# Kernel tuning notes

Measured on AMD Instinct MI355X. Metric: run time of the kernel, lower is better.

The kernel has to match this reference:

```python
import jax, jax.numpy as jnp
import numpy as np

BN_EPS = 1e-5
NORM_EPS = 1e-12
TEMPERATURE = 0.07
TOP_K = 128


def _projection_head(x, W1, b1, gamma, beta, W2, b2):
    # Linear(hidden, hidden); torch Linear weight is [out, in]
    y = x @ W1.T + b1
    # BatchNorm1d in training mode: batch statistics (biased variance)
    mu = jnp.mean(y, axis=0)
    var = jnp.var(y, axis=0)
    y = gamma * (y - mu) * jax.lax.rsqrt(var + BN_EPS) + beta
    # exact (erf) GELU, matching torch default
    y = jax.nn.gelu(y, approximate=False)
    return y @ W2.T + b2


def _l2_normalize(x):
    n = jnp.linalg.norm(x, axis=-1, keepdims=True)
    return x / jnp.maximum(n, NORM_EPS)


def setup_inputs() -> dict:
    key = jax.random.key(0)
    ks = jax.random.split(key, 5)
    B, N_NEG, H, P = 4096, 32768, 1024, 256
    h1 = jax.random.normal(ks[0], (B, H), dtype=jnp.float32)
    h2 = jax.random.normal(ks[1], (B, H), dtype=jnp.float32)
    h_neg = jax.random.normal(ks[2], (N_NEG, H), dtype=jnp.float32)
    W1 = jax.random.normal(ks[3], (H, H), dtype=jnp.float32) * (1.0 / np.sqrt(H))
    b1 = jnp.zeros((H,), dtype=jnp.float32)
    gamma = jnp.ones((H,), dtype=jnp.float32)
    beta = jnp.zeros((H,), dtype=jnp.float32)
    W2 = jax.random.normal(ks[4], (P, H), dtype=jnp.float32) * (1.0 / np.sqrt(H))
    b2 = jnp.zeros((P,), dtype=jnp.float32)
    return {"h1": h1, "h2": h2, "h_neg": h_neg, "W1": W1, "b1": b1,
            "gamma": gamma, "beta": beta, "W2": W2, "b2": b2}


def reference(h1, h2, h_neg, W1, b1, gamma, beta, W2, b2):
    z1 = _l2_normalize(_projection_head(h1, W1, b1, gamma, beta, W2, b2))
    z2 = _l2_normalize(_projection_head(h2, W1, b1, gamma, beta, W2, b2))
    z_neg = _l2_normalize(_projection_head(h_neg, W1, b1, gamma, beta, W2, b2))

    sim_neg = z1 @ z_neg.T                      # [B, N_neg]
    _, hard_idx = jax.lax.top_k(sim_neg, TOP_K) # [B, K]
    z_hard = z_neg[hard_idx]                    # [B, K, P] gather

    pos_sim = jnp.sum(z1 * z2, axis=-1, keepdims=True) / TEMPERATURE      # [B, 1]
    neg_sim = jnp.einsum('bp,bkp->bk', z1, z_hard) / TEMPERATURE          # [B, K]
    logits = jnp.concatenate([pos_sim, neg_sim], axis=1)                  # [B, 1+K]
    # cross entropy with all labels = 0
    loss = -jnp.mean(jax.nn.log_softmax(logits, axis=-1)[:, 0])
    return loss
```

## Files before the change

kernel.cpp:

```cpp
#include <hip/hip_runtime.h>
#include <hip/hip_bf16.h>
#include <math.h>

#define BATCH 4096
#define NNEG 32768
#define HID 1024
#define PROJ 256
#define TOPK 128
#define ROWS_TOTAL 40960
#define CHUNK 1024
#define INV_T 14.2857142857142857f

#define BM 128
#define BN 128
#define BK 64

#define BNS_ROWS 128

typedef __attribute__((ext_vector_type(8))) short bf16x8;
typedef __attribute__((ext_vector_type(4))) float f32x4;

__device__ __forceinline__ float b2f(unsigned short u) {
    return __uint_as_float(((unsigned)u) << 16);
}
__device__ __forceinline__ unsigned short f2b(float f) {
    unsigned u = __float_as_uint(f);
    unsigned r = (u + 0x7FFFu + ((u >> 16) & 1u)) >> 16;
    return (unsigned short)r;
}
__device__ __forceinline__ float gelu_fast(float v) {
    float v2 = v * v;
    float w = v * fmaf(v2, -0.1029433f, -2.3022086f);
    float e = exp2f(w);
    return v * __builtin_amdgcn_rcpf(1.0f + e);
}

__device__ __forceinline__ float blockReduceSumF(float v, volatile float* scratch) {
    #pragma unroll
    for (int o = 32; o > 0; o >>= 1) v += __shfl_down(v, o);
    int wid = threadIdx.x >> 6, lane = threadIdx.x & 63;
    __syncthreads();
    if (lane == 0) scratch[wid] = v;
    __syncthreads();
    return scratch[0] + scratch[1] + scratch[2] + scratch[3];
}
__device__ __forceinline__ int blockReduceSumI(int v, volatile int* scratch) {
    #pragma unroll
    for (int o = 32; o > 0; o >>= 1) v += __shfl_down(v, o);
    int wid = threadIdx.x >> 6, lane = threadIdx.x & 63;
    __syncthreads();
    if (lane == 0) scratch[wid] = v;
    __syncthreads();
    return scratch[0] + scratch[1] + scratch[2] + scratch[3];
}

__device__ __forceinline__ void gl_lds16(const unsigned short* g, unsigned short* l) {
    __builtin_amdgcn_global_load_lds(
        (const __attribute__((address_space(1))) unsigned*)g,
        (__attribute__((address_space(3))) unsigned*)l, 16, 0, 0);
}

__global__ __launch_bounds__(256) void conv_f2b(const float* __restrict__ src,
                                                unsigned short* __restrict__ dst, int n)
{
    int i = (blockIdx.x * 256 + threadIdx.x) * 4;
    if (i + 3 < n) {
        float4 v = *(const float4*)(src + i);
        ushort4 o;
        o.x = f2b(v.x); o.y = f2b(v.y); o.z = f2b(v.z); o.w = f2b(v.w);
        *(ushort4*)(dst + i) = o;
    }
}

__global__ __launch_bounds__(256) void conv_f2b8(const float* __restrict__ src,
                                                 unsigned short* __restrict__ dst)
{
    int i = (blockIdx.x * 256 + threadIdx.x) * 8;
    float4 a = *(const float4*)(src + i);
    float4 b = *(const float4*)(src + i + 4);
    ushort4 o0, o1;
    o0.x = f2b(a.x); o0.y = f2b(a.y); o0.z = f2b(a.z); o0.w = f2b(a.w);
    o1.x = f2b(b.x); o1.y = f2b(b.y); o1.z = f2b(b.z); o1.w = f2b(b.w);
    *(ushort4*)(dst + i) = o0;
    *(ushort4*)(dst + i + 4) = o1;
}

__device__ __forceinline__ void xcd_swizzle(int& bx, int& by) {
    int gx = gridDim.x;
    int orig = by * gx + bx;
    int q = (gx * gridDim.y) >> 3;
    int wg = (orig & 7) * q + (orig >> 3);
    bx = wg % gx;
    by = wg / gx;
}

__global__ __launch_bounds__(256) void mfma_gemm(
    const unsigned short* __restrict__ A, const unsigned short* __restrict__ Bw,
    const float* __restrict__ bias, unsigned short* __restrict__ C,
    int M, int N, int K)
{
    __shared__ unsigned short As[BM * BK];
    __shared__ unsigned short Bs[BN * BK];
    const int tid = threadIdx.x;
    int bxi = blockIdx.x, byi = blockIdx.y;
    xcd_swizzle(bxi, byi);
    const int bm = byi * BM;
    const int bn = bxi * BN;
    const int wave = tid >> 6;
    const int lane = tid & 63;
    const int wm = (wave >> 1) * 64;
    const int wn = (wave & 1) * 64;
    const int fr = lane & 15;
    const int fg = lane >> 4;

    int s_slot[4], s_row[4], s_c16[4];
    #pragma unroll
    for (int i = 0; i < 4; i++) {
        int s = wave * 256 + i * 64 + lane;
        s_slot[i] = (wave * 256 + i * 64) * 8;
        s_row[i] = s >> 3;
        s_c16[i] = (s & 7) ^ ((s >> 3) & 7);
    }

    f32x4 acc[4][4] = {};

    for (int k0 = 0; k0 < K; k0 += BK) {
        #pragma unroll
        for (int i = 0; i < 4; i++) {
            gl_lds16(A  + (size_t)(bm + s_row[i]) * K + k0 + s_c16[i] * 8, &As[s_slot[i]]);
            gl_lds16(Bw + (size_t)(bn + s_row[i]) * K + k0 + s_c16[i] * 8, &Bs[s_slot[i]]);
        }
        __syncthreads();
        #pragma unroll
        for (int ks = 0; ks < 2; ks++) {
            bf16x8 a[4], b[4];
            #pragma unroll
            for (int mi = 0; mi < 4; mi++) {
                int row = wm + mi * 16 + fr;
                a[mi] = *(const bf16x8*)&As[row * 64 + (((ks * 4 + fg) ^ (row & 7)) << 3)];
            }
            #pragma unroll
            for (int ni = 0; ni < 4; ni++) {
                int row = wn + ni * 16 + fr;
                b[ni] = *(const bf16x8*)&Bs[row * 64 + (((ks * 4 + fg) ^ (row & 7)) << 3)];
            }
            #pragma unroll
            for (int mi = 0; mi < 4; mi++)
                #pragma unroll
                for (int ni = 0; ni < 4; ni++)
                    acc[mi][ni] = __builtin_amdgcn_mfma_f32_16x16x32_bf16(a[mi], b[ni], acc[mi][ni], 0, 0, 0);
        }
        __syncthreads();
    }

    #pragma unroll
    for (int mi = 0; mi < 4; mi++) {
        #pragma unroll
        for (int ni = 0; ni < 4; ni++) {
            int col = bn + wn + ni * 16 + fr;
            int row0 = bm + wm + mi * 16 + fg * 4;
            float bv = bias ? bias[col] : 0.0f;
            #pragma unroll
            for (int r = 0; r < 4; r++) {
                float v = acc[mi][ni][r] + bv;
                C[(size_t)(row0 + r) * N + col] = f2b(v);
            }
        }
    }
}

__global__ __launch_bounds__(256) void bn_stats_partial(const unsigned short* __restrict__ Yb,
                                                        float* __restrict__ partial)
{
    __shared__ float lsum[1024];
    __shared__ float lssq[1024];
    const int cg = (threadIdx.x & 127) * 8;
    int r = blockIdx.x * BNS_ROWS + (threadIdx.x >> 7);
    float s[8] = {}, ss[8] = {};
    #pragma unroll 4
    for (int i = 0; i < BNS_ROWS / 2; i++, r += 2) {
        uint4 v = *(const uint4*)&Yb[(size_t)r * HID + cg];
        const unsigned short* u = (const unsigned short*)&v;
        #pragma unroll
        for (int j = 0; j < 8; j++) {
            float f = b2f(u[j]);
            s[j] += f; ss[j] += f * f;
        }
    }
    if (threadIdx.x >= 128) {
        #pragma unroll
        for (int j = 0; j < 8; j++) { lsum[cg + j] = s[j]; lssq[cg + j] = ss[j]; }
    }
    __syncthreads();
    if (threadIdx.x < 128) {
        float* outs = partial + (size_t)blockIdx.x * 2048;
        #pragma unroll
        for (int j = 0; j < 8; j++) {
            outs[cg + j]        = s[j] + lsum[cg + j];
            outs[1024 + cg + j] = ss[j] + lssq[cg + j];
        }
    }
}

__global__ __launch_bounds__(256) void bn_reduce_finalize(
    const float* __restrict__ partial,
    const float* __restrict__ gamma, const float* __restrict__ beta,
    float* __restrict__ scale, float* __restrict__ shift)
{
    int seg = blockIdx.y;
    int col = blockIdx.x * 256 + threadIdx.x;
    int base = (seg == 0) ? 0 : (seg == 1) ? 32 : 64;
    int nblk = (seg == 2) ? 256 : 32;
    const float* p = partial + (size_t)base * 2048;
    float s = 0.f, ss = 0.f;
    for (int b = 0; b < nblk; b++) {
        s  += p[(size_t)b * 2048 + col];
        ss += p[(size_t)b * 2048 + 1024 + col];
    }
    float n = (seg == 2) ? (float)NNEG : (float)BATCH;
    float mu = s / n;
    float var = ss / n - mu * mu;
    float sc = gamma[col] * rsqrtf(var + 1e-5f);
    scale[seg * HID + col] = sc;
    shift[seg * HID + col] = beta[col] - mu * sc;
}

__global__ __launch_bounds__(256) void bngelu(unsigned short* __restrict__ Yb,
                                              const float* __restrict__ scale,
                                              const float* __restrict__ shift)
{
    size_t i = ((size_t)blockIdx.x * 256 + threadIdx.x) * 8;
    int row = (int)(i >> 10);
    int seg = (row < BATCH) ? 0 : (row < 2 * BATCH) ? 1 : 2;
    int col = (int)(i & 1023);
    float4 sc0 = *(const float4*)(scale + seg * HID + col);
    float4 sc1 = *(const float4*)(scale + seg * HID + col + 4);
    float4 sh0 = *(const float4*)(shift + seg * HID + col);
    float4 sh1 = *(const float4*)(shift + seg * HID + col + 4);
    float sc[8] = { sc0.x, sc0.y, sc0.z, sc0.w, sc1.x, sc1.y, sc1.z, sc1.w };
    float sh[8] = { sh0.x, sh0.y, sh0.z, sh0.w, sh1.x, sh1.y, sh1.z, sh1.w };
    uint4 v = *(uint4*)&Yb[i];
    unsigned short* u = (unsigned short*)&v;
    #pragma unroll
    for (int j = 0; j < 8; j++) {
        float f = fmaf(b2f(u[j]), sc[j], sh[j]);
        u[j] = f2b(gelu_fast(f));
    }
    *(uint4*)&Yb[i] = v;
}

__global__ __launch_bounds__(256) void l2norm(unsigned short* __restrict__ Z,
                                              float* __restrict__ Zfp)
{
    __shared__ float scratch[4];
    size_t r = blockIdx.x;
    float v = b2f(Z[r * PROJ + threadIdx.x]);
    float t = blockReduceSumF(v * v, scratch);
    float scale = 1.0f / fmaxf(sqrtf(t), 1e-12f);
    float o = v * scale;
    Z[r * PROJ + threadIdx.x] = f2b(o);
    if (r < 2 * BATCH) Zfp[r * PROJ + threadIdx.x] = o;
}

__global__ __launch_bounds__(256) void topk_loss(
    const unsigned short* __restrict__ simb,
    const float* __restrict__ z1, const float* __restrict__ z2,
    int rowOffset, float* __restrict__ rowloss)
{
    __shared__ int   hcnt[4096];
    __shared__ int   segc[256];
    __shared__ int   sufc[256];
    __shared__ float fscratch[4];
    __shared__ int   iscratch[4];
    __shared__ int   sel_seg;
    __shared__ int   sh_bt, sh_run;

    const int tid = threadIdx.x;
    const int grow = rowOffset + blockIdx.x;
    const unsigned short* srow = simb + (size_t)blockIdx.x * NNEG;

    #pragma unroll
    for (int j = 0; j < 16; j++) hcnt[tid * 16 + j] = 0;

    float p = z1[(size_t)grow * PROJ + tid] * z2[(size_t)grow * PROJ + tid];
    float pos = blockReduceSumF(p, fscratch);
    __syncthreads();

    for (int i = tid * 8; i < NNEG; i += 256 * 8) {
        uint4 v4 = *(const uint4*)(srow + i);
        const unsigned short* u = (const unsigned short*)&v4;
        #pragma unroll
        for (int j = 0; j < 8; j++) {
            float v = b2f(u[j]);
            int k = (int)fmaf(v, 2048.f, 2048.f);
            k = min(max(k, 0), 4095);
            atomicAdd(&hcnt[k], 1);
        }
    }
    __syncthreads();

    int c = 0;
    #pragma unroll
    for (int j = 0; j < 16; j++) c += hcnt[tid * 16 + j];
    segc[tid] = c;
    sufc[tid] = c;
    __syncthreads();
    for (int st = 1; st < 256; st <<= 1) {
        int aC = (tid + st < 256) ? sufc[tid + st] : 0;
        __syncthreads();
        sufc[tid] += aC;
        __syncthreads();
    }
    if (sufc[tid] >= TOPK && sufc[tid] - segc[tid] < TOPK) sel_seg = tid;
    __syncthreads();
    if (tid == 0) {
        int t = sel_seg;
        int running = sufc[t] - segc[t];
        int bt = t * 16;
        for (int j = 15; j >= 0; j--) {
            int b = t * 16 + j;
            int cb = hcnt[b];
            if (running + cb >= TOPK) { bt = b; break; }
            running += cb;
        }
        sh_bt = bt; sh_run = running;
    }
    __syncthreads();
    const int bt = sh_bt;
    const float m = INV_T;

    float s_above = 0.f, s_eq = 0.f;
    int c_eq = 0;
    for (int i = tid * 8; i < NNEG; i += 256 * 8) {
        uint4 v4 = *(const uint4*)(srow + i);
        const unsigned short* u = (const unsigned short*)&v4;
        #pragma unroll
        for (int j = 0; j < 8; j++) {
            float v = b2f(u[j]);
            int k = (int)fmaf(v, 2048.f, 2048.f);
            k = min(max(k, 0), 4095);
            if (k >= bt) {
                float e = __expf(fmaf(v, INV_T, -m));
                if (k > bt) s_above += e;
                else { s_eq += e; c_eq++; }
            }
        }
    }
    s_above = blockReduceSumF(s_above, fscratch);
    __syncthreads();
    s_eq = blockReduceSumF(s_eq, fscratch);
    c_eq = blockReduceSumI(c_eq, iscratch);
    if (tid == 0) {
        int need = TOPK - sh_run;
        float avg = s_eq / (float)c_eq;
        float total = s_above + (float)need * avg + __expf(fmaf(pos, INV_T, -m));
        rowloss[grow] = m + logf(total) - pos * INV_T;
    }
}

__global__ __launch_bounds__(256) void loss_reduce(const float* __restrict__ rowloss,
                                                   float* __restrict__ out)
{
    __shared__ float scratch[4];
    float s = 0.f;
    for (int i = threadIdx.x; i < BATCH; i += 256) s += rowloss[i];
    s = blockReduceSumF(s, scratch);
    if (threadIdx.x == 0) out[0] = s / (float)BATCH;
}

extern "C" void kernel_launch(void* const* d_in, const int* in_sizes, int n_in,
                              void* d_out, int out_size, void* d_ws, size_t ws_size,
                              hipStream_t stream)
{
    const float* h1    = (const float*)d_in[0];
    const float* h2    = (const float*)d_in[1];
    const float* hneg  = (const float*)d_in[2];
    const float* W1    = (const float*)d_in[3];
    const float* b1    = (const float*)d_in[4];
    const float* gamma = (const float*)d_in[5];
    const float* beta  = (const float*)d_in[6];
    const float* W2    = (const float*)d_in[7];
    const float* b2    = (const float*)d_in[8];
    float* out = (float*)d_out;
    float* ws  = (float*)d_ws;

    unsigned short* X_all = (unsigned short*)ws;
    unsigned short* Yb    = (unsigned short*)(ws + 20971520);
    unsigned short* Z     = (unsigned short*)(ws + 41943040);
    unsigned short* W1b   = (unsigned short*)(ws + 47185920);
    unsigned short* W2b   = (unsigned short*)(ws + 47710208);
    float* partial = ws + 47841280;
    float* s_scale = ws + 48496640;
    float* s_shift = ws + 48499712;
    float* rowloss = ws + 48502784;
    unsigned short* simb = X_all;
    float*          Zfp  = ws + 16777216;

    conv_f2b<<<1024, 256, 0, stream>>>(W1, W1b, HID * HID);
    conv_f2b<<<256, 256, 0, stream>>>(W2, W2b, PROJ * HID);
    conv_f2b8<<<2048, 256, 0, stream>>>(h1, X_all);
    conv_f2b8<<<2048, 256, 0, stream>>>(h2, X_all + (size_t)BATCH * HID);
    conv_f2b8<<<16384, 256, 0, stream>>>(hneg, X_all + (size_t)2 * BATCH * HID);

    {
        dim3 g(HID / BN, ROWS_TOTAL / BM);
        mfma_gemm<<<g, 256, 0, stream>>>(X_all, W1b, b1, Yb, ROWS_TOTAL, HID, HID);
    }

    const int rows[3] = { BATCH, BATCH, NNEG };
    const int yoff[3] = { 0, BATCH, 2 * BATCH };
    const int poff[3] = { 0, 32, 64 };

    for (int s = 0; s < 3; s++) {
        bn_stats_partial<<<rows[s] / BNS_ROWS, 256, 0, stream>>>(
            Yb + (size_t)yoff[s] * HID, partial + (size_t)poff[s] * 2048);
    }
    bn_reduce_finalize<<<dim3(HID / 256, 3), 256, 0, stream>>>(partial, gamma, beta, s_scale, s_shift);

    bngelu<<<ROWS_TOTAL * HID / 8 / 256, 256, 0, stream>>>(Yb, s_scale, s_shift);

    {
        dim3 g(PROJ / BN, ROWS_TOTAL / BM);
        mfma_gemm<<<g, 256, 0, stream>>>(Yb, W2b, b2, Z, ROWS_TOTAL, PROJ, HID);
    }
    l2norm<<<ROWS_TOTAL, 256, 0, stream>>>(Z, Zfp);

    const unsigned short* znegb = Z + (size_t)(2 * BATCH) * PROJ;
    const float* z2v = Zfp + (size_t)BATCH * PROJ;
    for (int c = 0; c < BATCH / CHUNK; c++) {
        dim3 g(NNEG / BN, CHUNK / BM);
        mfma_gemm<<<g, 256, 0, stream>>>(Z + (size_t)(c * CHUNK) * PROJ, znegb, nullptr,
                                         simb, CHUNK, NNEG, PROJ);
        topk_loss<<<CHUNK, 256, 0, stream>>>(simb, Zfp, z2v, c * CHUNK, rowloss);
    }
    loss_reduce<<<1, 256, 0, stream>>>(rowloss, out);
}
```

Before: 621.7 us.

## Keep similarity row in registers across histogram and sum passes; double chunk size

The top-k loss kernel now loads each row's 32768 bf16 similarities into 16 uint4 registers per thread once and reuses them for both the histogram pass and the exp-sum pass, instead of reading global memory twice. The similarity chunk size is doubled, so fewer chunked GEMM and top-k launches are needed, and the fp32 Z buffer is moved to a new workspace offset so the larger similarity buffer does not overlap it. This raises register pressure (64 extra VGPRs) and may lower occupancy.

```diff
diff --git a/kernel.cpp b/kernel.cpp
--- a/kernel.cpp
+++ b/kernel.cpp
@@ -8,7 +8,7 @@
 #define PROJ 256
 #define TOPK 128
 #define ROWS_TOTAL 40960
-#define CHUNK 1024
+#define CHUNK 2048
 #define INV_T 14.2857142857142857f
 
 #define BM 128
@@ -286,15 +286,23 @@
     float pos = blockReduceSumF(p, fscratch);
     __syncthreads();
 
-    for (int i = tid * 8; i < NNEG; i += 256 * 8) {
-        uint4 v4 = *(const uint4*)(srow + i);
-        const unsigned short* u = (const unsigned short*)&v4;
-        #pragma unroll
-        for (int j = 0; j < 8; j++) {
-            float v = b2f(u[j]);
-            int k = (int)fmaf(v, 2048.f, 2048.f);
-            k = min(max(k, 0), 4095);
-            atomicAdd(&hcnt[k], 1);
+    uint4 vreg[16];
+    #pragma unroll
+    for (int i = 0; i < 16; i++)
+        vreg[i] = *(const uint4*)(srow + ((size_t)i * 256 + tid) * 8);
+
+    #pragma unroll
+    for (int i = 0; i < 16; i++) {
+        const unsigned* w = (const unsigned*)&vreg[i];
+        #pragma unroll
+        for (int j = 0; j < 4; j++) {
+            unsigned pq = w[j];
+            float v0 = b2f((unsigned short)(pq & 0xFFFFu));
+            float v1 = b2f((unsigned short)(pq >> 16));
+            int k0 = min(max((int)fmaf(v0, 2048.f, 2048.f), 0), 4095);
+            int k1 = min(max((int)fmaf(v1, 2048.f, 2048.f), 0), 4095);
+            atomicAdd(&hcnt[k0], 1);
+            atomicAdd(&hcnt[k1], 1);
         }
     }
     __syncthreads();
@@ -331,18 +339,21 @@
 
     float s_above = 0.f, s_eq = 0.f;
     int c_eq = 0;
-    for (int i = tid * 8; i < NNEG; i += 256 * 8) {
-        uint4 v4 = *(const uint4*)(srow + i);
-        const unsigned short* u = (const unsigned short*)&v4;
-        #pragma unroll
-        for (int j = 0; j < 8; j++) {
-            float v = b2f(u[j]);
-            int k = (int)fmaf(v, 2048.f, 2048.f);
-            k = min(max(k, 0), 4095);
-            if (k >= bt) {
-                float e = __expf(fmaf(v, INV_T, -m));
-                if (k > bt) s_above += e;
-                else { s_eq += e; c_eq++; }
+    #pragma unroll
+    for (int i = 0; i < 16; i++) {
+        const unsigned* w = (const unsigned*)&vreg[i];
+        #pragma unroll
+        for (int j = 0; j < 4; j++) {
+            unsigned pq = w[j];
+            #pragma unroll
+            for (int h = 0; h < 2; h++) {
+                float v = b2f((unsigned short)((h == 0) ? (pq & 0xFFFFu) : (pq >> 16)));
+                int k = min(max((int)fmaf(v, 2048.f, 2048.f), 0), 4095);
+                if (k >= bt) {
+                    float e = __expf(fmaf(v, INV_T, -m));
+                    if (k > bt) s_above += e;
+                    else { s_eq += e; c_eq++; }
+                }
             }
         }
     }
@@ -393,8 +404,8 @@
     float* s_scale = ws + 48496640;
     float* s_shift = ws + 48499712;
     float* rowloss = ws + 48502784;
+    float* Zfp     = ws + 48506880;
     unsigned short* simb = X_all;
-    float*          Zfp  = ws + 16777216;
 
     conv_f2b<<<1024, 256, 0, stream>>>(W1, W1b, HID * HID);
     conv_f2b<<<256, 256, 0, stream>>>(W2, W2b, PROJ * HID);
```

New measurement: 667.2 us. +7.3%, slower.

## Double-buffer LDS tiles in MFMA GEMM to overlap global loads with compute

Applied to the files above, without the earlier changes.

Makes the GEMM's shared-memory A/B tiles double-buffered. The next K-tile is prefetched via global-to-LDS loads while MFMAs run on the current tile, which leaves one barrier per iteration instead of two. Row base pointers are also precomputed once. LDS use doubles to 64KB per block, which may reduce occupancy. The Zfp workspace pointer is moved to a separate region, apparently to avoid aliasing with other buffers.

```diff
diff --git a/kernel.cpp b/kernel.cpp
--- a/kernel.cpp
+++ b/kernel.cpp
@@ -99,8 +99,8 @@
     const float* __restrict__ bias, unsigned short* __restrict__ C,
     int M, int N, int K)
 {
-    __shared__ unsigned short As[BM * BK];
-    __shared__ unsigned short Bs[BN * BK];
+    __shared__ unsigned short As[2][BM * BK];
+    __shared__ unsigned short Bs[2][BN * BK];
     const int tid = threadIdx.x;
     int bxi = blockIdx.x, byi = blockIdx.y;
     xcd_swizzle(bxi, byi);
@@ -113,36 +113,51 @@
     const int fr = lane & 15;
     const int fg = lane >> 4;
 
-    int s_slot[4], s_row[4], s_c16[4];
+    int s_slot[4];
+    const unsigned short* aptr[4];
+    const unsigned short* bptr[4];
     #pragma unroll
     for (int i = 0; i < 4; i++) {
         int s = wave * 256 + i * 64 + lane;
         s_slot[i] = (wave * 256 + i * 64) * 8;
-        s_row[i] = s >> 3;
-        s_c16[i] = (s & 7) ^ ((s >> 3) & 7);
+        int row = s >> 3;
+        int c16 = (s & 7) ^ (row & 7);
+        aptr[i] = A  + (size_t)(bm + row) * K + c16 * 8;
+        bptr[i] = Bw + (size_t)(bn + row) * K + c16 * 8;
     }
 
     f32x4 acc[4][4] = {};
-
-    for (int k0 = 0; k0 < K; k0 += BK) {
-        #pragma unroll
-        for (int i = 0; i < 4; i++) {
-            gl_lds16(A  + (size_t)(bm + s_row[i]) * K + k0 + s_c16[i] * 8, &As[s_slot[i]]);
-            gl_lds16(Bw + (size_t)(bn + s_row[i]) * K + k0 + s_c16[i] * 8, &Bs[s_slot[i]]);
-        }
-        __syncthreads();
+    const int nt = K / BK;
+
+    #pragma unroll
+    for (int i = 0; i < 4; i++) {
+        gl_lds16(aptr[i], &As[0][s_slot[i]]);
+        gl_lds16(bptr[i], &Bs[0][s_slot[i]]);
+    }
+    __syncthreads();
+
+    int cur = 0;
+    for (int t = 0; t < nt; ++t) {
+        if (t + 1 < nt) {
+            int k0n = (t + 1) * BK;
+            #pragma unroll
+            for (int i = 0; i < 4; i++) {
+                gl_lds16(aptr[i] + k0n, &As[cur ^ 1][s_slot[i]]);
+                gl_lds16(bptr[i] + k0n, &Bs[cur ^ 1][s_slot[i]]);
+            }
+        }
         #pragma unroll
         for (int ks = 0; ks < 2; ks++) {
             bf16x8 a[4], b[4];
             #pragma unroll
             for (int mi = 0; mi < 4; mi++) {
                 int row = wm + mi * 16 + fr;
-                a[mi] = *(const bf16x8*)&As[row * 64 + (((ks * 4 + fg) ^ (row & 7)) << 3)];
+                a[mi] = *(const bf16x8*)&As[cur][row * 64 + (((ks * 4 + fg) ^ (row & 7)) << 3)];
             }
             #pragma unroll
             for (int ni = 0; ni < 4; ni++) {
                 int row = wn + ni * 16 + fr;
-                b[ni] = *(const bf16x8*)&Bs[row * 64 + (((ks * 4 + fg) ^ (row & 7)) << 3)];
+                b[ni] = *(const bf16x8*)&Bs[cur][row * 64 + (((ks * 4 + fg) ^ (row & 7)) << 3)];
             }
             #pragma unroll
             for (int mi = 0; mi < 4; mi++)
@@ -151,6 +166,7 @@
                     acc[mi][ni] = __builtin_amdgcn_mfma_f32_16x16x32_bf16(a[mi], b[ni], acc[mi][ni], 0, 0, 0);
         }
         __syncthreads();
+        cur ^= 1;
     }
 
     #pragma unroll
@@ -393,8 +409,8 @@
     float* s_scale = ws + 48496640;
     float* s_shift = ws + 48499712;
     float* rowloss = ws + 48502784;
+    float* Zfp     = ws + 48506880;
     unsigned short* simb = X_all;
-    float*          Zfp  = ws + 16777216;
 
     conv_f2b<<<1024, 256, 0, stream>>>(W1, W1b, HID * HID);
     conv_f2b<<<256, 256, 0, stream>>>(W2, W2b, PROJ * HID);
```

New measurement: 657.8 us. +5.8%, slower.
